# Kernel tuning notes

Hardware: AMD Instinct MI355X
Metric: run time of the kernel (lower is better)

The kernel has to match this reference:

```python
import jax, jax.numpy as jnp
import numpy as np

T = 8192        # tokens (batch*seq)
D = 1024        # d_model
H = 4096        # expert hidden = 4*d_model
E = 16          # num_expert
K = 2           # moe_top_k


def setup_inputs() -> dict:
    key = jax.random.key(0)
    ks = jax.random.split(key, 7)
    s_in = 1.0 / np.sqrt(D)
    s_h = 1.0 / np.sqrt(H)
    return {
        "moe_inp": jax.random.normal(ks[0], (T, D), dtype=jnp.float32),
        "Wg": jax.random.normal(ks[1], (D, E), dtype=jnp.float32) * s_in,
        "bg": jnp.zeros((E,), dtype=jnp.float32),
        "W1": jax.random.normal(ks[2], (E, D, H), dtype=jnp.float32) * s_in,
        "b1": jnp.zeros((E, H), dtype=jnp.float32),
        "W2": jax.random.normal(ks[3], (E, H, D), dtype=jnp.float32) * s_h,
        "b2": jnp.zeros((E, D), dtype=jnp.float32),
    }


def reference(moe_inp, Wg, bg, W1, b1, W2, b2):
    # --- NaiveGate: linear -> top-k -> softmax over selected logits ---
    logits = moe_inp @ Wg + bg                      # [T, E]
    topk_val, topk_idx = jax.lax.top_k(logits, K)   # [T, K]
    gate_score = jax.nn.softmax(topk_val, axis=-1)  # [T, K]

    # Per-(token, expert) combine weight: sum of gate scores of slots routed to e.
    # Equivalent to scatter(dispatch) -> expert MLP -> gather(combine) weighted sum.
    onehot = jax.nn.one_hot(topk_idx, E, dtype=moe_inp.dtype)  # [T, K, E]
    comb_w = jnp.einsum('tk,tke->te', gate_score, onehot)      # [T, E]

    out = jnp.zeros_like(moe_inp)
    for e in range(E):  # fixed small expert count
        h = jax.nn.relu(moe_inp @ W1[e] + b1[e])   # [T, H]
        y = h @ W2[e] + b2[e]                      # [T, D]
        out = out + comb_w[:, e:e + 1] * y
    return out
```

## Files before the change

kernel.cpp:

```cpp
#include <hip/hip_runtime.h>
#include <hip/hip_bf16.h>
#include <stdint.h>


#define Tn 8192
#define Dn 1024
#define Hn 4096
#define En 16

typedef __attribute__((ext_vector_type(8))) short bf16x8;
typedef __attribute__((ext_vector_type(4))) float f32x4;

__device__ __forceinline__ unsigned short f2bf(float f) {
    union { __hip_bfloat16 h; unsigned short u; } cv;
    cv.h = __float2bfloat16(f);
    return cv.u;
}

__device__ __forceinline__ void gload_lds16(const void* gptr, void* lptr) {
    __builtin_amdgcn_global_load_lds(
        (const __attribute__((address_space(1))) uint32_t*)gptr,
        (__attribute__((address_space(3))) uint32_t*)lptr, 16, 0, 0);
}

__device__ __forceinline__ int find_e(const int* __restrict__ mb, int gm) {
    int e = 0;
#pragma unroll
    for (int i = 1; i < En; i++) e += (mb[i] <= gm) ? 1 : 0;
    return e;
}

__device__ __forceinline__ void waitvm8() { asm volatile("s_waitcnt vmcnt(8)" ::: "memory"); }
__device__ __forceinline__ void waitvm4() { asm volatile("s_waitcnt vmcnt(4)" ::: "memory"); }
__device__ __forceinline__ void waitvm0() { asm volatile("s_waitcnt vmcnt(0)" ::: "memory"); }
__device__ __forceinline__ void waitlgkm0() { asm volatile("s_waitcnt lgkmcnt(0)" ::: "memory"); }
__device__ __forceinline__ void barrier_raw() { asm volatile("s_barrier" ::: "memory"); }

__global__ __launch_bounds__(256) void gate_kernel(
    const float* __restrict__ x, const float* __restrict__ Wg,
    const float* __restrict__ bg,
    int* cnt, int* tok_e, int* tok_pos, float* tok_w)
{
    int t = blockIdx.x;
    int tid = threadIdx.x;
    __shared__ float part[256][17];
    __shared__ float logits[16];

    float p[16];
#pragma unroll
    for (int e = 0; e < 16; e++) p[e] = 0.f;

    float4 xv = *reinterpret_cast<const float4*>(x + (size_t)t * Dn + tid * 4);
    float xs[4] = {xv.x, xv.y, xv.z, xv.w};
#pragma unroll
    for (int j = 0; j < 4; j++) {
        int row = tid * 4 + j;
        const float4* wrow = reinterpret_cast<const float4*>(Wg + (size_t)row * 16);
#pragma unroll
        for (int q = 0; q < 4; q++) {
            float4 w4 = wrow[q];
            p[q * 4 + 0] += xs[j] * w4.x;
            p[q * 4 + 1] += xs[j] * w4.y;
            p[q * 4 + 2] += xs[j] * w4.z;
            p[q * 4 + 3] += xs[j] * w4.w;
        }
    }
#pragma unroll
    for (int e = 0; e < 16; e++) part[tid][e] = p[e];
    __syncthreads();
    for (int off = 128; off > 0; off >>= 1) {
        if (tid < off) {
#pragma unroll
            for (int e = 0; e < 16; e++) part[tid][e] += part[tid + off][e];
        }
        __syncthreads();
    }
    if (tid < 16) logits[tid] = part[0][tid] + bg[tid];
    __syncthreads();
    if (tid == 0) {
        float v0 = -1e30f, v1 = -1e30f; int i0 = -1, i1 = -1;
        for (int e = 0; e < 16; e++) { float v = logits[e]; if (v > v0) { v0 = v; i0 = e; } }
        for (int e = 0; e < 16; e++) { if (e == i0) continue; float v = logits[e]; if (v > v1) { v1 = v; i1 = e; } }
        float ex = __expf(v1 - v0);
        float w0 = 1.f / (1.f + ex);
        float w1 = ex / (1.f + ex);
        int p0 = atomicAdd(&cnt[i0], 1);
        int p1 = atomicAdd(&cnt[i1], 1);
        tok_e[t * 2 + 0] = i0; tok_e[t * 2 + 1] = i1;
        tok_pos[t * 2 + 0] = p0; tok_pos[t * 2 + 1] = p1;
        tok_w[t * 2 + 0] = w0; tok_w[t * 2 + 1] = w1;
    }
}

__global__ void scan_kernel(const int* cnt, int* base, int* mb)
{
    if (threadIdx.x == 0 && blockIdx.x == 0) {
        int b = 0, m = 0;
        for (int e = 0; e < En; e++) {
            base[e] = b; mb[e] = m;
            b += cnt[e];
            m += (cnt[e] + 255) >> 8;
        }
        base[En] = b; mb[En] = m;
    }
}

__global__ __launch_bounds__(256) void gather_kernel(
    const float* __restrict__ x, const int* tok_e, const int* tok_pos,
    const int* base, unsigned short* xg)
{
    int t = blockIdx.x; int tid = threadIdx.x;
    int e0 = tok_e[2 * t], e1 = tok_e[2 * t + 1];
    int r0 = base[e0] + tok_pos[2 * t];
    int r1 = base[e1] + tok_pos[2 * t + 1];
    float4 v = *reinterpret_cast<const float4*>(x + (size_t)t * Dn + tid * 4);
    ushort4 u;
    u.x = f2bf(v.x); u.y = f2bf(v.y); u.z = f2bf(v.z); u.w = f2bf(v.w);
    *reinterpret_cast<ushort4*>(xg + (size_t)r0 * Dn + tid * 4) = u;
    *reinterpret_cast<ushort4*>(xg + (size_t)r1 * Dn + tid * 4) = u;
}

__global__ __launch_bounds__(512) void convT_kernel(
    const float* __restrict__ src, unsigned short* __restrict__ dst, int R, int C)
{
    int e = blockIdx.z;
    const float* s = src + (size_t)e * R * C;
    unsigned short* d = dst + (size_t)e * R * C;
    __shared__ float tile[64][65];
    int r0 = blockIdx.y * 64, c0 = blockIdx.x * 64;
    int tr = threadIdx.x >> 4;
    int tc4 = (threadIdx.x & 15) * 4;
    float4 v0 = *reinterpret_cast<const float4*>(s + (size_t)(r0 + tr) * C + c0 + tc4);
    float4 v1 = *reinterpret_cast<const float4*>(s + (size_t)(r0 + tr + 32) * C + c0 + tc4);
    tile[tr][tc4 + 0] = v0.x; tile[tr][tc4 + 1] = v0.y;
    tile[tr][tc4 + 2] = v0.z; tile[tr][tc4 + 3] = v0.w;
    tile[tr + 32][tc4 + 0] = v1.x; tile[tr + 32][tc4 + 1] = v1.y;
    tile[tr + 32][tc4 + 2] = v1.z; tile[tr + 32][tc4 + 3] = v1.w;
    __syncthreads();
    ushort4 u0, u1;
    u0.x = f2bf(tile[tc4 + 0][tr]);      u1.x = f2bf(tile[tc4 + 0][tr + 32]);
    u0.y = f2bf(tile[tc4 + 1][tr]);      u1.y = f2bf(tile[tc4 + 1][tr + 32]);
    u0.z = f2bf(tile[tc4 + 2][tr]);      u1.z = f2bf(tile[tc4 + 2][tr + 32]);
    u0.w = f2bf(tile[tc4 + 3][tr]);      u1.w = f2bf(tile[tc4 + 3][tr + 32]);
    *reinterpret_cast<ushort4*>(d + (size_t)(c0 + tr) * R + r0 + tc4) = u0;
    *reinterpret_cast<ushort4*>(d + (size_t)(c0 + tr + 32) * R + r0 + tc4) = u1;
}

template<bool G1>
__global__ __launch_bounds__(512, 2) void gemm8p_kernel(
    const unsigned short* __restrict__ Ag, const unsigned short* __restrict__ Bg,
    const float* __restrict__ bias, unsigned short* __restrict__ outb,
    float* __restrict__ outf, size_t ystride,
    const int* __restrict__ cnt, const int* __restrict__ base,
    const int* __restrict__ mb)
{
    constexpr int KDIM = G1 ? Dn : Hn;
    constexpr int KLEN = G1 ? Dn : (Hn / 2);
    constexpr int NOUT = G1 ? Hn : Dn;
    constexpr int NT = KLEN / 32;
    __shared__ unsigned short ldsA[4][256 * 32];
    __shared__ unsigned short ldsB[4][256 * 32];

    int bid = blockIdx.x;
    int xcd = bid & 7;
    int gm, ntile, kh;
    if constexpr (G1) {
        int k = bid >> 3;
        gm = k >> 1;
        ntile = xcd * 2 + (k & 1);
        kh = 0;
    } else {
        gm = bid >> 3;
        ntile = xcd >> 1;
        kh = xcd & 1;
    }
    if (gm >= mb[En]) return;
    int e = find_e(mb, gm);
    int mtile = gm - mb[e];
    int M_e = cnt[e];
    int m0 = mtile * 256, n0 = ntile * 256;
    int kbase = kh * KLEN;
    int rowbase0 = base[e] + m0;
    const unsigned short* Ab = Ag + (size_t)rowbase0 * KDIM + kbase;
    const unsigned short* Bb = Bg + (size_t)e * NOUT * KDIM + (size_t)n0 * KDIM + kbase;

    int tid = threadIdx.x;
    int lane = tid & 63;
    int wid = tid >> 6;
    int wr = wid >> 2, wc = wid & 3;
    int lr16 = lane & 15, lk = lane >> 4;

    int ja0 = tid;        int ra0 = ja0 >> 2; int ca0 = (ja0 & 3) ^ ((ra0 >> 1) & 3);
    int ja1 = tid + 512;  int ra1 = ja1 >> 2; int ca1 = (ja1 & 3) ^ ((ra1 >> 1) & 3);
    const unsigned short* aSrc0 = Ab + (size_t)ra0 * KDIM + ca0 * 8;
    const unsigned short* aSrc1 = Ab + (size_t)ra1 * KDIM + ca1 * 8;
    const unsigned short* bSrc0 = Bb + (size_t)ra0 * KDIM + ca0 * 8;
    const unsigned short* bSrc1 = Bb + (size_t)ra1 * KDIM + ca1 * 8;

    int aoff[8], boff[4];
#pragma unroll
    for (int m = 0; m < 8; m++) {
        int row = wr * 128 + m * 16 + lr16;
        aoff[m] = row * 32 + ((lk ^ ((row >> 1) & 3)) << 3);
    }
#pragma unroll
    for (int n = 0; n < 4; n++) {
        int row = wc * 64 + n * 16 + lr16;
        boff[n] = row * 32 + ((lk ^ ((row >> 1) & 3)) << 3);
    }

    f32x4 acc[8][4];
#pragma unroll
    for (int m = 0; m < 8; m++)
#pragma unroll
        for (int n = 0; n < 4; n++) acc[m][n] = (f32x4){0.f, 0.f, 0.f, 0.f};

    auto stageA = [&](int t) {
        char* sa = (char*)ldsA[t & 3];
        int k0 = t * 32;
        gload_lds16(aSrc0 + k0, sa + ja0 * 16);
        gload_lds16(aSrc1 + k0, sa + ja1 * 16);
    };
    auto stageB = [&](int t) {
        char* sb = (char*)ldsB[t & 3];
        int k0 = t * 32;
        gload_lds16(bSrc0 + k0, sb + ja0 * 16);
        gload_lds16(bSrc1 + k0, sb + ja1 * 16);
    };

    stageB(0); stageA(0);
    stageB(1); stageA(1);
    stageB(2); stageA(2);
    waitvm8();
    barrier_raw();

#pragma unroll 4
    for (int t = 0; t < NT; ++t) {
        const unsigned short* sa = ldsA[t & 3];
        const unsigned short* sb = ldsB[t & 3];
        bf16x8 a[4], b[4];
#pragma unroll
        for (int m = 0; m < 4; m++) a[m] = *(const bf16x8*)(sa + aoff[m]);
#pragma unroll
        for (int n = 0; n < 4; n++) b[n] = *(const bf16x8*)(sb + boff[n]);
        if (t + 3 < NT) stageB(t + 3);
        barrier_raw();
        waitlgkm0();
        __builtin_amdgcn_s_setprio(1);
#pragma unroll
        for (int m = 0; m < 4; m++)
#pragma unroll
            for (int n = 0; n < 4; n++)
                acc[m][n] = __builtin_amdgcn_mfma_f32_16x16x32_bf16(b[n], a[m], acc[m][n], 0, 0, 0);
        __builtin_amdgcn_s_setprio(0);
        barrier_raw();
#pragma unroll
        for (int m = 0; m < 4; m++) a[m] = *(const bf16x8*)(sa + aoff[m + 4]);
        if (t + 3 < NT) stageA(t + 3);
        barrier_raw();
        waitlgkm0();
        __builtin_amdgcn_s_setprio(1);
#pragma unroll
        for (int m = 0; m < 4; m++)
#pragma unroll
            for (int n = 0; n < 4; n++)
                acc[m + 4][n] = __builtin_amdgcn_mfma_f32_16x16x32_bf16(b[n], a[m], acc[m + 4][n], 0, 0, 0);
        __builtin_amdgcn_s_setprio(0);
        if (t < NT - 3)       waitvm8();
        else if (t == NT - 3) waitvm4();
        else if (t == NT - 2) waitvm0();
        barrier_raw();
    }

    bool addb = G1 || (kh == 0);
    const float* be = bias + (size_t)e * NOUT;
    int lj = (lane >> 4) * 4;
    float* yb = outf + (G1 ? 0 : (size_t)kh * ystride);
#pragma unroll
    for (int m = 0; m < 8; m++) {
        int rt = wr * 128 + m * 16 + lr16;
        if (m0 + rt < M_e) {
            size_t rowoff = (size_t)(rowbase0 + rt) * NOUT;
#pragma unroll
            for (int n = 0; n < 4; n++) {
                int col0 = n0 + wc * 64 + n * 16 + lj;
                float4 bs = addb ? *reinterpret_cast<const float4*>(be + col0)
                                 : (float4){0.f, 0.f, 0.f, 0.f};
                float v0 = acc[m][n][0] + bs.x;
                float v1 = acc[m][n][1] + bs.y;
                float v2 = acc[m][n][2] + bs.z;
                float v3 = acc[m][n][3] + bs.w;
                if constexpr (G1) {
                    ushort4 u;
                    u.x = f2bf(fmaxf(v0, 0.f));
                    u.y = f2bf(fmaxf(v1, 0.f));
                    u.z = f2bf(fmaxf(v2, 0.f));
                    u.w = f2bf(fmaxf(v3, 0.f));
                    *reinterpret_cast<ushort4*>(outb + rowoff + col0) = u;
                } else {
                    float4 o = {v0, v1, v2, v3};
                    *reinterpret_cast<float4*>(yb + rowoff + col0) = o;
                }
            }
        }
    }
}

__global__ __launch_bounds__(256) void combine_kernel(
    const float* __restrict__ y, size_t ystride,
    const int* __restrict__ tok_e, const int* __restrict__ tok_pos,
    const int* __restrict__ base, const float* __restrict__ tok_w,
    float* __restrict__ out)
{
    int t = blockIdx.x, tid = threadIdx.x;
    int e0 = tok_e[2 * t], e1 = tok_e[2 * t + 1];
    int r0 = base[e0] + tok_pos[2 * t];
    int r1 = base[e1] + tok_pos[2 * t + 1];
    float w0 = tok_w[2 * t], w1 = tok_w[2 * t + 1];
    const float* y1 = y + ystride;
    float4 a0 = *reinterpret_cast<const float4*>(y  + (size_t)r0 * Dn + tid * 4);
    float4 a1 = *reinterpret_cast<const float4*>(y1 + (size_t)r0 * Dn + tid * 4);
    float4 b0 = *reinterpret_cast<const float4*>(y  + (size_t)r1 * Dn + tid * 4);
    float4 b1 = *reinterpret_cast<const float4*>(y1 + (size_t)r1 * Dn + tid * 4);
    float4 o;
    o.x = w0 * (a0.x + a1.x) + w1 * (b0.x + b1.x);
    o.y = w0 * (a0.y + a1.y) + w1 * (b0.y + b1.y);
    o.z = w0 * (a0.z + a1.z) + w1 * (b0.z + b1.z);
    o.w = w0 * (a0.w + a1.w) + w1 * (b0.w + b1.w);
    *reinterpret_cast<float4*>(out + (size_t)t * Dn + tid * 4) = o;
}

extern "C" void kernel_launch(void* const* d_in, const int* in_sizes, int n_in,
                              void* d_out, int out_size, void* d_ws, size_t ws_size,
                              hipStream_t stream)
{
    const float* x  = (const float*)d_in[0];
    const float* Wg = (const float*)d_in[1];
    const float* bg = (const float*)d_in[2];
    const float* W1 = (const float*)d_in[3];
    const float* b1 = (const float*)d_in[4];
    const float* W2 = (const float*)d_in[5];
    const float* b2 = (const float*)d_in[6];
    float* out = (float*)d_out;

    char* ws = (char*)d_ws;
    size_t off = 0;
    auto alloc = [&](size_t bytes) {
        size_t o = off; off += (bytes + 255) & ~(size_t)255; return o;
    };
    const int ROWS = Tn * 2;
    const int RCAP = ROWS + 256;
    const size_t YSTR = (size_t)RCAP * Dn;

    unsigned short* Wt = (unsigned short*)(ws + alloc((size_t)En * Hn * Dn * 2));
    unsigned short* xg = (unsigned short*)(ws + alloc((size_t)RCAP * Dn * 2));
    unsigned short* hg = (unsigned short*)(ws + alloc((size_t)RCAP * Hn * 2));
    float* yv      = (float*)(ws + alloc(2 * YSTR * 4));
    int*   cnt     = (int*)(ws + alloc(En * 4));
    int*   base    = (int*)(ws + alloc((En + 1) * 4));
    int*   mb      = (int*)(ws + alloc((En + 1) * 4));
    int*   tok_e   = (int*)(ws + alloc(Tn * 2 * 4));
    int*   tok_pos = (int*)(ws + alloc(Tn * 2 * 4));
    float* tok_w   = (float*)(ws + alloc(Tn * 2 * 4));
    (void)ws_size; (void)in_sizes; (void)n_in; (void)out_size;

    hipMemsetAsync(cnt, 0, En * 4, stream);

    gate_kernel<<<Tn, 256, 0, stream>>>(x, Wg, bg, cnt, tok_e, tok_pos, tok_w);
    scan_kernel<<<1, 64, 0, stream>>>(cnt, base, mb);
    gather_kernel<<<Tn, 256, 0, stream>>>(x, tok_e, tok_pos, base, xg);

    convT_kernel<<<dim3(Hn / 64, Dn / 64, En), 512, 0, stream>>>(W1, Wt, Dn, Hn);
    gemm8p_kernel<true><<<1280, 512, 0, stream>>>(
        xg, Wt, b1, hg, nullptr, 0, cnt, base, mb);

    convT_kernel<<<dim3(Dn / 64, Hn / 64, En), 512, 0, stream>>>(W2, Wt, Hn, Dn);
    gemm8p_kernel<false><<<640, 512, 0, stream>>>(
        hg, Wt, b2, nullptr, yv, YSTR, cnt, base, mb);

    combine_kernel<<<Tn, 256, 0, stream>>>(yv, YSTR, tok_e, tok_pos, base, tok_w, out);
}
```

Baseline: 848.6 us.

## Make expert GEMMs persistent over tile rounds and batch gating 16 tokens per block

The grouped expert GEMMs now launch a fixed grid of 256 blocks that loop over M-tile rounds, replacing one-shot grids of 1280/640 blocks that often early-exit. This cuts idle or oversized launches and keeps the XCD-to-N-tile mapping fixed. The gate kernel now handles 16 tokens per block, with Wg staged transposed in LDS and top-2 selected by a 16-lane shuffle reduction instead of a shared-memory tree reduction. The risk is that the persistent loop serialises tiles per block with a pipeline prologue/drain each round and may leave CUs idle at the tail.

```diff
diff --git a/kernel.cpp b/kernel.cpp
--- a/kernel.cpp
+++ b/kernel.cpp
@@ -36,56 +36,59 @@
 __device__ __forceinline__ void waitlgkm0() { asm volatile("s_waitcnt lgkmcnt(0)" ::: "memory"); }
 __device__ __forceinline__ void barrier_raw() { asm volatile("s_barrier" ::: "memory"); }
 
+__device__ __forceinline__ bool better(float va, int ia, float vb, int ib) {
+    return (va > vb) || (va == vb && ia < ib);
+}
+
 __global__ __launch_bounds__(256) void gate_kernel(
     const float* __restrict__ x, const float* __restrict__ Wg,
     const float* __restrict__ bg,
     int* cnt, int* tok_e, int* tok_pos, float* tok_w)
 {
-    int t = blockIdx.x;
+    __shared__ float wgt[16 * 1028];
     int tid = threadIdx.x;
-    __shared__ float part[256][17];
-    __shared__ float logits[16];
-
-    float p[16];
-#pragma unroll
-    for (int e = 0; e < 16; e++) p[e] = 0.f;
-
-    float4 xv = *reinterpret_cast<const float4*>(x + (size_t)t * Dn + tid * 4);
-    float xs[4] = {xv.x, xv.y, xv.z, xv.w};
-#pragma unroll
-    for (int j = 0; j < 4; j++) {
-        int row = tid * 4 + j;
-        const float4* wrow = reinterpret_cast<const float4*>(Wg + (size_t)row * 16);
-#pragma unroll
-        for (int q = 0; q < 4; q++) {
-            float4 w4 = wrow[q];
-            p[q * 4 + 0] += xs[j] * w4.x;
-            p[q * 4 + 1] += xs[j] * w4.y;
-            p[q * 4 + 2] += xs[j] * w4.z;
-            p[q * 4 + 3] += xs[j] * w4.w;
-        }
-    }
-#pragma unroll
-    for (int e = 0; e < 16; e++) part[tid][e] = p[e];
+    int t0 = blockIdx.x * 16;
+
+#pragma unroll
+    for (int i = 0; i < 64; i++) {
+        int idx = i * 256 + tid;
+        int k = idx >> 4, e = idx & 15;
+        wgt[e * 1028 + k] = Wg[idx];
+    }
     __syncthreads();
-    for (int off = 128; off > 0; off >>= 1) {
-        if (tid < off) {
-#pragma unroll
-            for (int e = 0; e < 16; e++) part[tid][e] += part[tid + off][e];
-        }
-        __syncthreads();
-    }
-    if (tid < 16) logits[tid] = part[0][tid] + bg[tid];
-    __syncthreads();
-    if (tid == 0) {
-        float v0 = -1e30f, v1 = -1e30f; int i0 = -1, i1 = -1;
-        for (int e = 0; e < 16; e++) { float v = logits[e]; if (v > v0) { v0 = v; i0 = e; } }
-        for (int e = 0; e < 16; e++) { if (e == i0) continue; float v = logits[e]; if (v > v1) { v1 = v; i1 = e; } }
+
+    int tok = tid >> 4, e = tid & 15;
+    const float4* xr = reinterpret_cast<const float4*>(x + (size_t)(t0 + tok) * Dn);
+    const float4* wr = reinterpret_cast<const float4*>(&wgt[e * 1028]);
+    float acc = 0.f;
+#pragma unroll 8
+    for (int q = 0; q < 256; q++) {
+        float4 xv = xr[q], wv = wr[q];
+        acc += xv.x * wv.x + xv.y * wv.y + xv.z * wv.z + xv.w * wv.w;
+    }
+    acc += bg[e];
+
+    float v0 = acc, v1 = -1e30f;
+    int i0 = e, i1 = -1;
+#pragma unroll
+    for (int m = 1; m < 16; m <<= 1) {
+        float ov0 = __shfl_xor(v0, m, 16); int oi0 = __shfl_xor(i0, m, 16);
+        float ov1 = __shfl_xor(v1, m, 16); int oi1 = __shfl_xor(i1, m, 16);
+        if (better(ov0, oi0, v0, i0)) {
+            if (better(v0, i0, ov1, oi1)) { v1 = v0; i1 = i0; }
+            else                          { v1 = ov1; i1 = oi1; }
+            v0 = ov0; i0 = oi0;
+        } else if (better(ov0, oi0, v1, i1)) {
+            v1 = ov0; i1 = oi0;
+        }
+    }
+    if (e == 0) {
         float ex = __expf(v1 - v0);
         float w0 = 1.f / (1.f + ex);
         float w1 = ex / (1.f + ex);
         int p0 = atomicAdd(&cnt[i0], 1);
         int p1 = atomicAdd(&cnt[i1], 1);
+        int t = t0 + tok;
         tok_e[t * 2 + 0] = i0; tok_e[t * 2 + 1] = i1;
         tok_pos[t * 2 + 0] = p0; tok_pos[t * 2 + 1] = p1;
         tok_w[t * 2 + 0] = w0; tok_w[t * 2 + 1] = w1;
@@ -163,39 +166,19 @@
 
     int bid = blockIdx.x;
     int xcd = bid & 7;
-    int gm, ntile, kh;
-    if constexpr (G1) {
-        int k = bid >> 3;
-        gm = k >> 1;
-        ntile = xcd * 2 + (k & 1);
-        kh = 0;
-    } else {
-        gm = bid >> 3;
-        ntile = xcd >> 1;
-        kh = xcd & 1;
-    }
-    if (gm >= mb[En]) return;
-    int e = find_e(mb, gm);
-    int mtile = gm - mb[e];
-    int M_e = cnt[e];
-    int m0 = mtile * 256, n0 = ntile * 256;
-    int kbase = kh * KLEN;
-    int rowbase0 = base[e] + m0;
-    const unsigned short* Ab = Ag + (size_t)rowbase0 * KDIM + kbase;
-    const unsigned short* Bb = Bg + (size_t)e * NOUT * KDIM + (size_t)n0 * KDIM + kbase;
+    int slot = bid >> 3;
+    int totalgm = mb[En];
+    int rounds = G1 ? ((totalgm + 15) >> 4) : ((totalgm + 31) >> 5);
 
     int tid = threadIdx.x;
     int lane = tid & 63;
     int wid = tid >> 6;
     int wr = wid >> 2, wc = wid & 3;
     int lr16 = lane & 15, lk = lane >> 4;
+    int lj = (lane >> 4) * 4;
 
     int ja0 = tid;        int ra0 = ja0 >> 2; int ca0 = (ja0 & 3) ^ ((ra0 >> 1) & 3);
     int ja1 = tid + 512;  int ra1 = ja1 >> 2; int ca1 = (ja1 & 3) ^ ((ra1 >> 1) & 3);
-    const unsigned short* aSrc0 = Ab + (size_t)ra0 * KDIM + ca0 * 8;
-    const unsigned short* aSrc1 = Ab + (size_t)ra1 * KDIM + ca1 * 8;
-    const unsigned short* bSrc0 = Bb + (size_t)ra0 * KDIM + ca0 * 8;
-    const unsigned short* bSrc1 = Bb + (size_t)ra1 * KDIM + ca1 * 8;
 
     int aoff[8], boff[4];
 #pragma unroll
@@ -209,97 +192,124 @@
         boff[n] = row * 32 + ((lk ^ ((row >> 1) & 3)) << 3);
     }
 
-    f32x4 acc[8][4];
-#pragma unroll
-    for (int m = 0; m < 8; m++)
-#pragma unroll
-        for (int n = 0; n < 4; n++) acc[m][n] = (f32x4){0.f, 0.f, 0.f, 0.f};
-
-    auto stageA = [&](int t) {
-        char* sa = (char*)ldsA[t & 3];
-        int k0 = t * 32;
-        gload_lds16(aSrc0 + k0, sa + ja0 * 16);
-        gload_lds16(aSrc1 + k0, sa + ja1 * 16);
-    };
-    auto stageB = [&](int t) {
-        char* sb = (char*)ldsB[t & 3];
-        int k0 = t * 32;
-        gload_lds16(bSrc0 + k0, sb + ja0 * 16);
-        gload_lds16(bSrc1 + k0, sb + ja1 * 16);
-    };
-
-    stageB(0); stageA(0);
-    stageB(1); stageA(1);
-    stageB(2); stageA(2);
-    waitvm8();
-    barrier_raw();
+    for (int r = 0; r < rounds; r++) {
+        int gm, ntile, kh;
+        if constexpr (G1) {
+            gm = r * 16 + (slot >> 1);
+            ntile = xcd * 2 + (slot & 1);
+            kh = 0;
+        } else {
+            gm = r * 32 + slot;
+            ntile = xcd >> 1;
+            kh = xcd & 1;
+        }
+        if (gm >= totalgm) continue;
+
+        int e = find_e(mb, gm);
+        int mtile = gm - mb[e];
+        int M_e = cnt[e];
+        int m0 = mtile * 256, n0 = ntile * 256;
+        int kbase = kh * KLEN;
+        int rowbase0 = base[e] + m0;
+        const unsigned short* Ab = Ag + (size_t)rowbase0 * KDIM + kbase;
+        const unsigned short* Bb = Bg + (size_t)e * NOUT * KDIM + (size_t)n0 * KDIM + kbase;
+
+        const unsigned short* aSrc0 = Ab + (size_t)ra0 * KDIM + ca0 * 8;
+        const unsigned short* aSrc1 = Ab + (size_t)ra1 * KDIM + ca1 * 8;
+        const unsigned short* bSrc0 = Bb + (size_t)ra0 * KDIM + ca0 * 8;
+        const unsigned short* bSrc1 = Bb + (size_t)ra1 * KDIM + ca1 * 8;
+
+        f32x4 acc[8][4];
+#pragma unroll
+        for (int m = 0; m < 8; m++)
+#pragma unroll
+            for (int n = 0; n < 4; n++) acc[m][n] = (f32x4){0.f, 0.f, 0.f, 0.f};
+
+        auto stageA = [&](int t) {
+            char* sa = (char*)ldsA[t & 3];
+            int k0 = t * 32;
+            gload_lds16(aSrc0 + k0, sa + ja0 * 16);
+            gload_lds16(aSrc1 + k0, sa + ja1 * 16);
+        };
+        auto stageB = [&](int t) {
+            char* sb = (char*)ldsB[t & 3];
+            int k0 = t * 32;
+            gload_lds16(bSrc0 + k0, sb + ja0 * 16);
+            gload_lds16(bSrc1 + k0, sb + ja1 * 16);
+        };
+
+        stageB(0); stageA(0);
+        stageB(1); stageA(1);
+        stageB(2); stageA(2);
+        waitvm8();
+        barrier_raw();
 
 #pragma unroll 4
-    for (int t = 0; t < NT; ++t) {
-        const unsigned short* sa = ldsA[t & 3];
-        const unsigned short* sb = ldsB[t & 3];
-        bf16x8 a[4], b[4];
-#pragma unroll
-        for (int m = 0; m < 4; m++) a[m] = *(const bf16x8*)(sa + aoff[m]);
-#pragma unroll
-        for (int n = 0; n < 4; n++) b[n] = *(const bf16x8*)(sb + boff[n]);
-        if (t + 3 < NT) stageB(t + 3);
-        barrier_raw();
-        waitlgkm0();
-        __builtin_amdgcn_s_setprio(1);
-#pragma unroll
-        for (int m = 0; m < 4; m++)
-#pragma unroll
-            for (int n = 0; n < 4; n++)
-                acc[m][n] = __builtin_amdgcn_mfma_f32_16x16x32_bf16(b[n], a[m], acc[m][n], 0, 0, 0);
-        __builtin_amdgcn_s_setprio(0);
-        barrier_raw();
-#pragma unroll
-        for (int m = 0; m < 4; m++) a[m] = *(const bf16x8*)(sa + aoff[m + 4]);
-        if (t + 3 < NT) stageA(t + 3);
-        barrier_raw();
-        waitlgkm0();
-        __builtin_amdgcn_s_setprio(1);
-#pragma unroll
-        for (int m = 0; m < 4; m++)
-#pragma unroll
-            for (int n = 0; n < 4; n++)
-                acc[m + 4][n] = __builtin_amdgcn_mfma_f32_16x16x32_bf16(b[n], a[m], acc[m + 4][n], 0, 0, 0);
-        __builtin_amdgcn_s_setprio(0);
-        if (t < NT - 3)       waitvm8();
-        else if (t == NT - 3) waitvm4();
-        else if (t == NT - 2) waitvm0();
-        barrier_raw();
-    }
-
-    bool addb = G1 || (kh == 0);
-    const float* be = bias + (size_t)e * NOUT;
-    int lj = (lane >> 4) * 4;
-    float* yb = outf + (G1 ? 0 : (size_t)kh * ystride);
-#pragma unroll
-    for (int m = 0; m < 8; m++) {
-        int rt = wr * 128 + m * 16 + lr16;
-        if (m0 + rt < M_e) {
-            size_t rowoff = (size_t)(rowbase0 + rt) * NOUT;
-#pragma unroll
-            for (int n = 0; n < 4; n++) {
-                int col0 = n0 + wc * 64 + n * 16 + lj;
-                float4 bs = addb ? *reinterpret_cast<const float4*>(be + col0)
-                                 : (float4){0.f, 0.f, 0.f, 0.f};
-                float v0 = acc[m][n][0] + bs.x;
-                float v1 = acc[m][n][1] + bs.y;
-                float v2 = acc[m][n][2] + bs.z;
-                float v3 = acc[m][n][3] + bs.w;
-                if constexpr (G1) {
-                    ushort4 u;
-                    u.x = f2bf(fmaxf(v0, 0.f));
-                    u.y = f2bf(fmaxf(v1, 0.f));
-                    u.z = f2bf(fmaxf(v2, 0.f));
-                    u.w = f2bf(fmaxf(v3, 0.f));
-                    *reinterpret_cast<ushort4*>(outb + rowoff + col0) = u;
-                } else {
-                    float4 o = {v0, v1, v2, v3};
-                    *reinterpret_cast<float4*>(yb + rowoff + col0) = o;
+        for (int t = 0; t < NT; ++t) {
+            const unsigned short* sa = ldsA[t & 3];
+            const unsigned short* sb = ldsB[t & 3];
+            bf16x8 a[4], b[4];
+#pragma unroll
+            for (int m = 0; m < 4; m++) a[m] = *(const bf16x8*)(sa + aoff[m]);
+#pragma unroll
+            for (int n = 0; n < 4; n++) b[n] = *(const bf16x8*)(sb + boff[n]);
+            if (t + 3 < NT) stageB(t + 3);
+            barrier_raw();
+            waitlgkm0();
+            __builtin_amdgcn_s_setprio(1);
+#pragma unroll
+            for (int m = 0; m < 4; m++)
+#pragma unroll
+                for (int n = 0; n < 4; n++)
+                    acc[m][n] = __builtin_amdgcn_mfma_f32_16x16x32_bf16(b[n], a[m], acc[m][n], 0, 0, 0);
+            __builtin_amdgcn_s_setprio(0);
+            barrier_raw();
+#pragma unroll
+            for (int m = 0; m < 4; m++) a[m] = *(const bf16x8*)(sa + aoff[m + 4]);
+            if (t + 3 < NT) stageA(t + 3);
+            barrier_raw();
+            waitlgkm0();
+            __builtin_amdgcn_s_setprio(1);
+#pragma unroll
+            for (int m = 0; m < 4; m++)
+#pragma unroll
+                for (int n = 0; n < 4; n++)
+                    acc[m + 4][n] = __builtin_amdgcn_mfma_f32_16x16x32_bf16(b[n], a[m], acc[m + 4][n], 0, 0, 0);
+            __builtin_amdgcn_s_setprio(0);
+            if (t < NT - 3)       waitvm8();
+            else if (t == NT - 3) waitvm4();
+            else if (t == NT - 2) waitvm0();
+            barrier_raw();
+        }
+
+        bool addb = G1 || (kh == 0);
+        const float* be = bias + (size_t)e * NOUT;
+        float* yb = outf + (G1 ? 0 : (size_t)kh * ystride);
+#pragma unroll
+        for (int m = 0; m < 8; m++) {
+            int rt = wr * 128 + m * 16 + lr16;
+            if (m0 + rt < M_e) {
+                size_t rowoff = (size_t)(rowbase0 + rt) * NOUT;
+#pragma unroll
+                for (int n = 0; n < 4; n++) {
+                    int col0 = n0 + wc * 64 + n * 16 + lj;
+                    float4 bs = addb ? *reinterpret_cast<const float4*>(be + col0)
+                                     : (float4){0.f, 0.f, 0.f, 0.f};
+                    float v0 = acc[m][n][0] + bs.x;
+                    float v1 = acc[m][n][1] + bs.y;
+                    float v2 = acc[m][n][2] + bs.z;
+                    float v3 = acc[m][n][3] + bs.w;
+                    if constexpr (G1) {
+                        ushort4 u;
+                        u.x = f2bf(fmaxf(v0, 0.f));
+                        u.y = f2bf(fmaxf(v1, 0.f));
+                        u.z = f2bf(fmaxf(v2, 0.f));
+                        u.w = f2bf(fmaxf(v3, 0.f));
+                        *reinterpret_cast<ushort4*>(outb + rowoff + col0) = u;
+                    } else {
+                        float4 o = {v0, v1, v2, v3};
+                        *reinterpret_cast<float4*>(yb + rowoff + col0) = o;
+                    }
                 }
             }
         }
@@ -366,16 +376,16 @@
 
     hipMemsetAsync(cnt, 0, En * 4, stream);
 
-    gate_kernel<<<Tn, 256, 0, stream>>>(x, Wg, bg, cnt, tok_e, tok_pos, tok_w);
+    gate_kernel<<<Tn / 16, 256, 0, stream>>>(x, Wg, bg, cnt, tok_e, tok_pos, tok_w);
     scan_kernel<<<1, 64, 0, stream>>>(cnt, base, mb);
     gather_kernel<<<Tn, 256, 0, stream>>>(x, tok_e, tok_pos, base, xg);
 
     convT_kernel<<<dim3(Hn / 64, Dn / 64, En), 512, 0, stream>>>(W1, Wt, Dn, Hn);
-    gemm8p_kernel<true><<<1280, 512, 0, stream>>>(
+    gemm8p_kernel<true><<<256, 512, 0, stream>>>(
         xg, Wt, b1, hg, nullptr, 0, cnt, base, mb);
 
     convT_kernel<<<dim3(Dn / 64, Hn / 64, En), 512, 0, stream>>>(W2, Wt, Hn, Dn);
-    gemm8p_kernel<false><<<640, 512, 0, stream>>>(
+    gemm8p_kernel<false><<<256, 512, 0, stream>>>(
         hg, Wt, b2, nullptr, yv, YSTR, cnt, base, mb);
 
     combine_kernel<<<Tn, 256, 0, stream>>>(yv, YSTR, tok_e, tok_pos, base, tok_w, out);
```

New measurement: 737.2 us. -13.1%, faster.
